# Optimization experiments

Measured on AMD Instinct MI355X. Metric: run time of the kernel, lower is better.

The kernel has to match this reference:

```python
import jax, jax.numpy as jnp
import numpy as np

N_PULSES = 64
BATCH = 16384
N_STATES = 21


def setup_inputs() -> dict:
    key = jax.random.key(0)
    k = jax.random.split(key, 6)
    flip_angles = jax.random.uniform(k[0], (N_PULSES,), jnp.float32) * jnp.pi          # 0..pi rad
    phases = jax.random.uniform(k[1], (N_PULSES,), jnp.float32) * 2.0 * jnp.pi         # 0..2pi rad
    T1 = 500.0 + 1000.0 * jax.random.uniform(k[2], (BATCH,), jnp.float32)
    T2 = 50.0 + 100.0 * jax.random.uniform(k[3], (BATCH,), jnp.float32)
    B0 = 50.0 * jax.random.normal(k[4], (BATCH,), jnp.float32)                         # Hz
    B1 = 0.8 + 0.4 * jax.random.uniform(k[5], (BATCH,), jnp.float32)                   # unitless
    return {"flip_angles": flip_angles, "phases": phases, "T1": T1, "T2": T2,
            "B0": B0, "B1": B1, "TR": 500, "TE": 10}


def _epg_forward(flip_angles, phases, T1, T2, B0, B1, TR):
    B = T1.shape[0]
    E1 = jnp.exp(-TR / T1)[:, None]                 # (B,1)
    E2 = jnp.exp(-TR / T2)[:, None]                 # (B,1)
    phi = (2.0 * jnp.pi * B0 * TR / 1000.0)[:, None]
    eb0p = jnp.exp(1j * phi.astype(jnp.complex64))  # (B,1) complex64
    eb0m = jnp.conj(eb0p)
    B1c = B1[:, None]

    Fp0 = jnp.zeros((B, N_STATES), jnp.complex64)
    Fm0 = jnp.zeros((B, N_STATES), jnp.complex64)
    Z0 = jnp.zeros((B, N_STATES), jnp.float32).at[:, 0].set(1.0)

    def step(carry, ab):
        Fp, Fm, Z = carry
        a, b = ab
        # relax
        Fp = E2 * Fp
        Fm = E2 * Fm
        Z = (E1 * Z).at[:, 0].add(1.0 - E1[:, 0])
        # B0 dephasing
        Fp = Fp * eb0p
        Fm = Fm * eb0m
        # RF rotation (B1-scaled flip angle)
        alpha = a * B1c                              # (B,1)
        ca = jnp.cos(alpha / 2)
        sa = jnp.sin(alpha / 2)
        eib = jnp.exp(1j * b.astype(jnp.complex64))  # scalar
        emib = jnp.conj(eib)
        Zc = Z.astype(jnp.complex64)
        Fp_n = ca**2 * Fp + sa**2 * jnp.conj(Fm) * eib**2 + 1j * ca * sa * (Zc * eib)
        Fm_n = sa**2 * jnp.conj(Fp) * emib**2 + ca**2 * Fm - 1j * ca * sa * (Zc * emib)
        Z_n = (-1j * sa * ca * (Fp * emib - Fm * eib) + (ca**2 - sa**2) * Zc).real
        # gradient shift
        Fp_s = jnp.roll(Fp_n, 1, axis=1).at[:, 0].set(0)
        Fm_s = jnp.roll(Fm_n, -1, axis=1).at[:, -1].set(0)
        out = jnp.stack([Fp_s.real, Fp_s.imag, Fm_s.real, Fm_s.imag, Z_n], axis=0)
        return (Fp_s, Fm_s, Z_n), out

    _, outs = jax.lax.scan(step, (Fp0, Fm0, Z0), (flip_angles, phases))
    return outs  # (N, 5, B, S): [Fp.re, Fp.im, Fm.re, Fm.im, Z] per pulse


def reference(flip_angles, phases, T1, T2, B0, B1, TR, TE):
    TRf = jnp.float32(TR)
    return _epg_forward(flip_angles, phases, T1, T2, B0, B1, TRf)
```

## Files before the change

### kernel.cpp

```cpp
#include <hip/hip_runtime.h>

namespace {
constexpr int NP      = 64;
constexpr int BATCH_N = 16384;
constexpr int NS      = 21;
constexpr int BPB     = 12;
constexpr int CHAN    = BATCH_N * NS;
constexpr unsigned CHANB = (unsigned)CHAN * 4u;
constexpr unsigned STEPB = 5u * CHANB;
constexpr int LDSF    = BPB * NS * 5;
constexpr int NSLOT   = (LDSF + 3) / 4;
}

__global__ __launch_bounds__(256) void epg_kernel(
    const float* __restrict__ flip, const float* __restrict__ ph,
    const float* __restrict__ T1,   const float* __restrict__ T2,
    const float* __restrict__ B0,   const float* __restrict__ B1,
    const int*   __restrict__ TRp,  float* __restrict__ out)
{
  __shared__ __align__(16) float lds[2][LDSF];

  const int tid  = threadIdx.x;
  const int lane = tid & 63;
  const int wv   = tid >> 6;
  const int sub  = lane / 21;
  const int s    = lane - sub * 21;
  const int bg   = blockIdx.x * BPB + wv * 3 + sub;
  const bool active = (sub < 3) && (bg < BATCH_N);
  const int  bs  = active ? bg : 0;
  const int  inner = wv * 63 + lane;

  const int rem = min(BPB, BATCH_N - blockIdx.x * BPB);
  const unsigned base0 = (unsigned)blockIdx.x * (BPB * NS * 4u);
  int      loff[2]; unsigned goff[2]; bool fdo[2];
  #pragma unroll
  for (int k = 0; k < 2; ++k) {
    const int i = tid + k * 256;
    const int c = i / 63;
    const int j = i - c * 63;
    fdo[k]  = (i < NSLOT) && (4 * j < rem * NS);
    loff[k] = c * (BPB * NS) + 4 * j;
    goff[k] = base0 + (unsigned)c * CHANB + (unsigned)j * 16u;
  }

  const float TR = (float)TRp[0];
  const float E1 = __expf(-TR / T1[bs]);
  const float E2 = __expf(-TR / T2[bs]);
  const float b1 = B1[bs];
  const float rec = (s == 0) ? (1.0f - E1) : 0.0f;
  const float phi = 6.283185307179586f * 0.001f * TR * B0[bs];
  float bi, br; __sincosf(phi, &bi, &br);

  float fpr = 0.f, fpi = 0.f, fmr = 0.f, fmi = 0.f;
  float z = (s == 0) ? 1.0f : 0.0f;

  char* const outb = (char*)out;
  unsigned pbase = 0;
  int buf = 0;

  for (int p = 0; p < NP; ++p) {
    const float a = flip[p];
    const float b = ph[p];
    float sa, ca; __sincosf(0.5f * a * b1, &sa, &ca);
    float ei, er; __sincosf(b, &ei, &er);
    const float w2r = er * er - ei * ei;
    const float w2i = 2.0f * er * ei;
    const float c2 = ca * ca, s2 = sa * sa, cs = ca * sa;

    fpr *= E2; fpi *= E2; fmr *= E2; fmi *= E2;
    z = E1 * z + rec;

    {
      float t = fpr * br - fpi * bi;
      fpi = fpr * bi + fpi * br; fpr = t;
      float u = fmr * br + fmi * bi;
      fmi = fmi * br - fmr * bi; fmr = u;
    }

    const float zcs = cs * z;
    const float fpnr =  c2 * fpr + s2 * (fmr * w2r + fmi * w2i) - zcs * ei;
    const float fpni =  c2 * fpi + s2 * (fmr * w2i - fmi * w2r) + zcs * er;
    const float fmnr =  c2 * fmr + s2 * (fpr * w2r - fpi * w2i) - zcs * ei;
    const float fmni =  c2 * fmi - s2 * (fpr * w2i + fpi * w2r) - zcs * er;
    const float zn   =  cs * ((fpi - fmi) * er - (fpr + fmr) * ei)
                        + (c2 - s2) * z;

    const float ufpr = __shfl_up(fpnr, 1);
    const float ufpi = __shfl_up(fpni, 1);
    const float dfmr = __shfl_down(fmnr, 1);
    const float dfmi = __shfl_down(fmni, 1);
    fpr = (s == 0)  ? 0.f : ufpr;
    fpi = (s == 0)  ? 0.f : ufpi;
    fmr = (s == 20) ? 0.f : dfmr;
    fmi = (s == 20) ? 0.f : dfmi;
    z = zn;

    if (active) {
      float* lb = lds[buf];
      lb[inner]                = fpr;
      lb[BPB * NS + inner]     = fpi;
      lb[2 * BPB * NS + inner] = fmr;
      lb[3 * BPB * NS + inner] = fmi;
      lb[4 * BPB * NS + inner] = zn;
    }
    __syncthreads();

    {
      const float* lb = lds[buf];
      #pragma unroll
      for (int k = 0; k < 2; ++k) {
        if (fdo[k]) {
          const float4 v = *(const float4*)&lb[loff[k]];
          *(float4*)(outb + pbase + goff[k]) = v;
        }
      }
    }
    buf ^= 1;
    pbase += STEPB;
  }
}

extern "C" void kernel_launch(void* const* d_in, const int* in_sizes, int n_in,
                              void* d_out, int out_size, void* d_ws, size_t ws_size,
                              hipStream_t stream) {
  const float* flip = (const float*)d_in[0];
  const float* ph   = (const float*)d_in[1];
  const float* T1   = (const float*)d_in[2];
  const float* T2   = (const float*)d_in[3];
  const float* B0   = (const float*)d_in[4];
  const float* B1   = (const float*)d_in[5];
  const int*   TR   = (const int*)d_in[6];
  float* out = (float*)d_out;

  const int blocks = (BATCH_N + BPB - 1) / BPB;
  epg_kernel<<<blocks, 256, 0, stream>>>(flip, ph, T1, T2, B0, B1, TR, out);
}
```

Baseline: 521.1 us.

## Write outputs directly from registers and precompute per-pulse phase table in LDS

Removes the per-pulse LDS staging buffer and block-wide barrier, so each lane stores its five state values straight to global memory with scalar stores. Those stores are still coalesced, because each wave's 63 active lanes cover contiguous addresses. Per-pulse phase sin/cos and its square are computed once per block into a small shared table and read back each step, and the loop is unrolled by two. The cost is scalar 4-byte stores in place of float4 stores, but the per-step __syncthreads goes away and waves can run ahead of each other.

After: 518.0 us. Within noise of the previous version (-0.6%).

```diff
diff --git a/kernel.cpp b/kernel.cpp
--- a/kernel.cpp
+++ b/kernel.cpp
@@ -8,8 +8,6 @@
 constexpr int CHAN    = BATCH_N * NS;
 constexpr unsigned CHANB = (unsigned)CHAN * 4u;
 constexpr unsigned STEPB = 5u * CHANB;
-constexpr int LDSF    = BPB * NS * 5;
-constexpr int NSLOT   = (LDSF + 3) / 4;
 }
 
 __global__ __launch_bounds__(256) void epg_kernel(
@@ -18,9 +16,21 @@
     const float* __restrict__ B0,   const float* __restrict__ B1,
     const int*   __restrict__ TRp,  float* __restrict__ out)
 {
-  __shared__ __align__(16) float lds[2][LDSF];
+  __shared__ __align__(16) float tbl[NP][8];
 
   const int tid  = threadIdx.x;
+
+  if (tid < NP) {
+    const float a = flip[tid];
+    const float b = ph[tid];
+    float ei, er; __sincosf(b, &ei, &er);
+    tbl[tid][0] = a;
+    tbl[tid][1] = er;
+    tbl[tid][2] = ei;
+    tbl[tid][3] = er * er - ei * ei;
+    tbl[tid][4] = 2.0f * er * ei;
+  }
+
   const int lane = tid & 63;
   const int wv   = tid >> 6;
   const int sub  = lane / 21;
@@ -28,20 +38,6 @@
   const int bg   = blockIdx.x * BPB + wv * 3 + sub;
   const bool active = (sub < 3) && (bg < BATCH_N);
   const int  bs  = active ? bg : 0;
-  const int  inner = wv * 63 + lane;
-
-  const int rem = min(BPB, BATCH_N - blockIdx.x * BPB);
-  const unsigned base0 = (unsigned)blockIdx.x * (BPB * NS * 4u);
-  int      loff[2]; unsigned goff[2]; bool fdo[2];
-  #pragma unroll
-  for (int k = 0; k < 2; ++k) {
-    const int i = tid + k * 256;
-    const int c = i / 63;
-    const int j = i - c * 63;
-    fdo[k]  = (i < NSLOT) && (4 * j < rem * NS);
-    loff[k] = c * (BPB * NS) + 4 * j;
-    goff[k] = base0 + (unsigned)c * CHANB + (unsigned)j * 16u;
-  }
 
   const float TR = (float)TRp[0];
   const float E1 = __expf(-TR / T1[bs]);
@@ -54,17 +50,24 @@
   float fpr = 0.f, fpi = 0.f, fmr = 0.f, fmi = 0.f;
   float z = (s == 0) ? 1.0f : 0.0f;
 
-  char* const outb = (char*)out;
-  unsigned pbase = 0;
-  int buf = 0;
+  char* const o0 = (char*)out;
+  char* const o1 = o0 + CHANB;
+  char* const o2 = o0 + 2u * CHANB;
+  char* const o3 = o0 + 3u * CHANB;
+  char* const o4 = o0 + 4u * CHANB;
+  unsigned off = (unsigned)(bg * NS + s) * 4u;
 
+  __syncthreads();
+
+  #pragma unroll 2
   for (int p = 0; p < NP; ++p) {
-    const float a = flip[p];
-    const float b = ph[p];
+    const float4 tq = *(const float4*)&tbl[p][0];
+    const float a   = tq.x;
+    const float er  = tq.y, ei  = tq.z;
+    const float w2r = tq.w;
+    const float w2i = tbl[p][4];
+
     float sa, ca; __sincosf(0.5f * a * b1, &sa, &ca);
-    float ei, er; __sincosf(b, &ei, &er);
-    const float w2r = er * er - ei * ei;
-    const float w2i = 2.0f * er * ei;
     const float c2 = ca * ca, s2 = sa * sa, cs = ca * sa;
 
     fpr *= E2; fpi *= E2; fmr *= E2; fmi *= E2;
@@ -96,27 +99,13 @@
     z = zn;
 
     if (active) {
-      float* lb = lds[buf];
-      lb[inner]                = fpr;
-      lb[BPB * NS + inner]     = fpi;
-      lb[2 * BPB * NS + inner] = fmr;
-      lb[3 * BPB * NS + inner] = fmi;
-      lb[4 * BPB * NS + inner] = zn;
+      *(float*)(o0 + off) = fpr;
+      *(float*)(o1 + off) = fpi;
+      *(float*)(o2 + off) = fmr;
+      *(float*)(o3 + off) = fmi;
+      *(float*)(o4 + off) = zn;
     }
-    __syncthreads();
-
-    {
-      const float* lb = lds[buf];
-      #pragma unroll
-      for (int k = 0; k < 2; ++k) {
-        if (fdo[k]) {
-          const float4 v = *(const float4*)&lb[loff[k]];
-          *(float4*)(outb + pbase + goff[k]) = v;
-        }
-      }
-    }
-    buf ^= 1;
-    pbase += STEPB;
+    off += STEPB;
   }
 }
 
```

## Use 16 batches per block, precompute pulse table in LDS, nontemporal stores

Applied to the files above, without the earlier changes.

Widens each block to 384 threads covering 16 batch items, so each per-channel output row is 84 float4s with no tail handling and the grid divides evenly. Per-pulse phase trig and flip/phase loads move into a shared table computed once per block. Output stores become nontemporal to skip cache pollution, and the pulse loop is unrolled by two. The trade-off is higher LDS use and a larger block, which can lower occupancy, and nontemporal stores change cache behaviour in ways that are hard to predict.

New measurement: 453.4 us. -13.0%, faster.

```diff
diff --git a/kernel.cpp b/kernel.cpp
--- a/kernel.cpp
+++ b/kernel.cpp
@@ -4,51 +4,65 @@
 constexpr int NP      = 64;
 constexpr int BATCH_N = 16384;
 constexpr int NS      = 21;
-constexpr int BPB     = 12;
+constexpr int BPB     = 16;
 constexpr int CHAN    = BATCH_N * NS;
 constexpr unsigned CHANB = (unsigned)CHAN * 4u;
 constexpr unsigned STEPB = 5u * CHANB;
 constexpr int LDSF    = BPB * NS * 5;
-constexpr int NSLOT   = (LDSF + 3) / 4;
+constexpr int NSLOT   = LDSF / 4;
+constexpr int TPB     = 384;
+typedef float vf4 __attribute__((ext_vector_type(4)));
 }
 
-__global__ __launch_bounds__(256) void epg_kernel(
+__global__ __launch_bounds__(TPB) void epg_kernel(
     const float* __restrict__ flip, const float* __restrict__ ph,
     const float* __restrict__ T1,   const float* __restrict__ T2,
     const float* __restrict__ B0,   const float* __restrict__ B1,
     const int*   __restrict__ TRp,  float* __restrict__ out)
 {
   __shared__ __align__(16) float lds[2][LDSF];
+  __shared__ __align__(16) float tbl[NP][8];
 
   const int tid  = threadIdx.x;
+
+  if (tid < NP) {
+    const float a = flip[tid];
+    const float b = ph[tid];
+    float ei, er; __sincosf(b, &ei, &er);
+    tbl[tid][0] = a;
+    tbl[tid][1] = er;
+    tbl[tid][2] = ei;
+    tbl[tid][3] = er * er - ei * ei;
+    tbl[tid][4] = 2.0f * er * ei;
+  }
+
   const int lane = tid & 63;
   const int wv   = tid >> 6;
   const int sub  = lane / 21;
   const int s    = lane - sub * 21;
-  const int bg   = blockIdx.x * BPB + wv * 3 + sub;
-  const bool active = (sub < 3) && (bg < BATCH_N);
-  const int  bs  = active ? bg : 0;
-  const int  inner = wv * 63 + lane;
+  const int idx  = wv * 3 + sub;
+  const bool active = (sub < 3) && (idx < BPB);
+  const int  bg  = blockIdx.x * BPB + (active ? idx : 0);
+  const int  inner = idx * NS + s;
 
-  const int rem = min(BPB, BATCH_N - blockIdx.x * BPB);
   const unsigned base0 = (unsigned)blockIdx.x * (BPB * NS * 4u);
   int      loff[2]; unsigned goff[2]; bool fdo[2];
   #pragma unroll
   for (int k = 0; k < 2; ++k) {
-    const int i = tid + k * 256;
-    const int c = i / 63;
-    const int j = i - c * 63;
-    fdo[k]  = (i < NSLOT) && (4 * j < rem * NS);
+    const int i = tid + k * TPB;
+    const int c = i / 84;
+    const int j = i - c * 84;
+    fdo[k]  = (i < NSLOT);
     loff[k] = c * (BPB * NS) + 4 * j;
     goff[k] = base0 + (unsigned)c * CHANB + (unsigned)j * 16u;
   }
 
   const float TR = (float)TRp[0];
-  const float E1 = __expf(-TR / T1[bs]);
-  const float E2 = __expf(-TR / T2[bs]);
-  const float b1 = B1[bs];
+  const float E1 = __expf(-TR / T1[bg]);
+  const float E2 = __expf(-TR / T2[bg]);
+  const float b1 = B1[bg];
   const float rec = (s == 0) ? (1.0f - E1) : 0.0f;
-  const float phi = 6.283185307179586f * 0.001f * TR * B0[bs];
+  const float phi = 6.283185307179586f * 0.001f * TR * B0[bg];
   float bi, br; __sincosf(phi, &bi, &br);
 
   float fpr = 0.f, fpi = 0.f, fmr = 0.f, fmi = 0.f;
@@ -58,13 +72,17 @@
   unsigned pbase = 0;
   int buf = 0;
 
+  __syncthreads();
+
+  #pragma unroll 2
   for (int p = 0; p < NP; ++p) {
-    const float a = flip[p];
-    const float b = ph[p];
+    const vf4 tq = *(const vf4*)&tbl[p][0];
+    const float a   = tq.x;
+    const float er  = tq.y, ei  = tq.z;
+    const float w2r = tq.w;
+    const float w2i = tbl[p][4];
+
     float sa, ca; __sincosf(0.5f * a * b1, &sa, &ca);
-    float ei, er; __sincosf(b, &ei, &er);
-    const float w2r = er * er - ei * ei;
-    const float w2i = 2.0f * er * ei;
     const float c2 = ca * ca, s2 = sa * sa, cs = ca * sa;
 
     fpr *= E2; fpi *= E2; fmr *= E2; fmi *= E2;
@@ -110,8 +128,8 @@
       #pragma unroll
       for (int k = 0; k < 2; ++k) {
         if (fdo[k]) {
-          const float4 v = *(const float4*)&lb[loff[k]];
-          *(float4*)(outb + pbase + goff[k]) = v;
+          const vf4 v = *(const vf4*)&lb[loff[k]];
+          __builtin_nontemporal_store(v, (vf4*)(outb + pbase + goff[k]));
         }
       }
     }
@@ -132,6 +150,6 @@
   const int*   TR   = (const int*)d_in[6];
   float* out = (float*)d_out;
 
-  const int blocks = (BATCH_N + BPB - 1) / BPB;
-  epg_kernel<<<blocks, 256, 0, stream>>>(flip, ph, T1, T2, B0, B1, TR, out);
+  const int blocks = BATCH_N / BPB;
+  epg_kernel<<<blocks, TPB, 0, stream>>>(flip, ph, T1, T2, B0, B1, TR, out);
 }
```
